# Kernel optimization log

Measured on AMD Instinct MI355X. Metric: run time of the kernel, lower is better.

## Reference

```python
import jax, jax.numpy as jnp
import numpy as np

BN_EPS = 1e-5


def _bn(h, gamma, beta, mean, var):
    return (h - mean) * jax.lax.rsqrt(var + BN_EPS) * gamma + beta


def _gin_conv(x, edge_index, edge_weight, Wa, ba, g, be, m, v, Wb, bb):
    # GINConv: (1+eps)*x + sum_j w_ij * x_j, eps=0; then MLP: Linear->BN->ReLU->Linear
    src, dst = edge_index[0], edge_index[1]
    msg = x[src] * edge_weight[:, None]                      # [E, C]
    agg = jax.ops.segment_sum(msg, dst, num_segments=x.shape[0])  # [N, C]
    h = x + agg
    h = h @ Wa + ba
    h = jax.nn.relu(_bn(h, g, be, m, v))
    return h @ Wb + bb


def setup_inputs() -> dict:
    key = jax.random.key(0)
    ks = jax.random.split(key, 16)
    N, E, C_IN, C_OUT, H = 100000, 1600000, 128, 64, 32
    x = jax.random.normal(ks[0], (N, C_IN), dtype=jnp.float32)
    edge_index = jax.random.randint(ks[1], (2, E), 0, N, dtype=jnp.int32)
    edge_weight = jax.random.uniform(ks[2], (E,), dtype=jnp.float32)
    s1 = 1.0 / np.sqrt(C_IN)
    s2 = 1.0 / np.sqrt(H)
    return {
        "x": x,
        "edge_weight": edge_weight,
        "W1a": jax.random.normal(ks[3], (C_IN, H), dtype=jnp.float32) * s1,
        "b1a": jnp.zeros((H,), jnp.float32),
        "g1": jnp.ones((H,), jnp.float32),
        "be1": jnp.zeros((H,), jnp.float32),
        "m1": jax.random.normal(ks[4], (H,), dtype=jnp.float32) * 0.1,
        "v1": jax.random.uniform(ks[5], (H,), dtype=jnp.float32) + 0.5,
        "W1b": jax.random.normal(ks[6], (H, H), dtype=jnp.float32) * s2,
        "b1b": jnp.zeros((H,), jnp.float32),
        "W2a": jax.random.normal(ks[7], (H, C_OUT), dtype=jnp.float32) * s2,
        "b2a": jnp.zeros((C_OUT,), jnp.float32),
        "g2": jnp.ones((C_OUT,), jnp.float32),
        "be2": jnp.zeros((C_OUT,), jnp.float32),
        "m2": jax.random.normal(ks[8], (C_OUT,), dtype=jnp.float32) * 0.1,
        "v2": jax.random.uniform(ks[9], (C_OUT,), dtype=jnp.float32) + 0.5,
        "W2b": jax.random.normal(ks[10], (C_OUT, C_OUT), dtype=jnp.float32) * (1.0 / np.sqrt(C_OUT)),
        "b2b": jnp.zeros((C_OUT,), jnp.float32),
        "edge_index": edge_index,
    }


def reference(x, edge_weight, W1a, b1a, g1, be1, m1, v1, W1b, b1b,
              W2a, b2a, g2, be2, m2, v2, W2b, b2b, edge_index):
    # eval mode: dropout(p=0.6) is identity, BN uses running stats
    h = jax.nn.relu(_gin_conv(x, edge_index, edge_weight,
                              W1a, b1a, g1, be1, m1, v1, W1b, b1b))
    out = _gin_conv(h, edge_index, edge_weight,
                    W2a, b2a, g2, be2, m2, v2, W2b, b2b)
    return out
```

## Files before the change

### kernel.cpp

```cpp
#include <hip/hip_runtime.h>


#define BN_EPS 1e-5f
#define BKT 128
#define BKT_SH 7
#define EPB 4096
#define MAXB 800
#define LDS_E 2560

__device__ __forceinline__ unsigned short f2bf(float f) {
    unsigned u = __float_as_uint(f);
    return (unsigned short)((u + 0x7FFFu + ((u >> 16) & 1u)) >> 16);
}
__device__ __forceinline__ float bflo(unsigned u) { return __uint_as_float(u << 16); }
__device__ __forceinline__ float bfhi(unsigned u) { return __uint_as_float(u & 0xFFFF0000u); }

__device__ __forceinline__ void gacc8(uint4 v, float w, float* acc) {
    acc[0] += bflo(v.x) * w; acc[1] += bfhi(v.x) * w;
    acc[2] += bflo(v.y) * w; acc[3] += bfhi(v.y) * w;
    acc[4] += bflo(v.z) * w; acc[5] += bfhi(v.z) * w;
    acc[6] += bflo(v.w) * w; acc[7] += bfhi(v.w) * w;
}

__device__ __forceinline__ void gather_seg8(const unsigned short* __restrict__ tab,
                                            const int2* __restrict__ epack,
                                            int e, int end, int c0, float* acc) {
    long long q0 = 0, q1 = 0, q2 = 0, q3 = 0;
    if (e + 4 <= end) {
        q0 = __builtin_nontemporal_load((const long long*)&epack[e + 0]);
        q1 = __builtin_nontemporal_load((const long long*)&epack[e + 1]);
        q2 = __builtin_nontemporal_load((const long long*)&epack[e + 2]);
        q3 = __builtin_nontemporal_load((const long long*)&epack[e + 3]);
    }
    for (; e + 8 <= end; e += 4) {
        int s0 = (int)q0, s1 = (int)q1, s2 = (int)q2, s3 = (int)q3;
        float w0 = __int_as_float((int)(q0 >> 32));
        float w1 = __int_as_float((int)(q1 >> 32));
        float w2 = __int_as_float((int)(q2 >> 32));
        float w3 = __int_as_float((int)(q3 >> 32));
        uint4 v0 = *(const uint4*)&tab[(size_t)s0 * 32 + c0];
        uint4 v1 = *(const uint4*)&tab[(size_t)s1 * 32 + c0];
        uint4 v2 = *(const uint4*)&tab[(size_t)s2 * 32 + c0];
        uint4 v3 = *(const uint4*)&tab[(size_t)s3 * 32 + c0];
        q0 = __builtin_nontemporal_load((const long long*)&epack[e + 4]);
        q1 = __builtin_nontemporal_load((const long long*)&epack[e + 5]);
        q2 = __builtin_nontemporal_load((const long long*)&epack[e + 6]);
        q3 = __builtin_nontemporal_load((const long long*)&epack[e + 7]);
        gacc8(v0, w0, acc); gacc8(v1, w1, acc);
        gacc8(v2, w2, acc); gacc8(v3, w3, acc);
    }
    if (e + 4 <= end) {
        int s0 = (int)q0, s1 = (int)q1, s2 = (int)q2, s3 = (int)q3;
        float w0 = __int_as_float((int)(q0 >> 32));
        float w1 = __int_as_float((int)(q1 >> 32));
        float w2 = __int_as_float((int)(q2 >> 32));
        float w3 = __int_as_float((int)(q3 >> 32));
        uint4 v0 = *(const uint4*)&tab[(size_t)s0 * 32 + c0];
        uint4 v1 = *(const uint4*)&tab[(size_t)s1 * 32 + c0];
        uint4 v2 = *(const uint4*)&tab[(size_t)s2 * 32 + c0];
        uint4 v3 = *(const uint4*)&tab[(size_t)s3 * 32 + c0];
        gacc8(v0, w0, acc); gacc8(v1, w1, acc);
        gacc8(v2, w2, acc); gacc8(v3, w3, acc);
        e += 4;
    }
    for (; e < end; ++e) {
        long long q = __builtin_nontemporal_load((const long long*)&epack[e]);
        int sn = (int)q;
        float w = __int_as_float((int)(q >> 32));
        uint4 v = *(const uint4*)&tab[(size_t)sn * 32 + c0];
        gacc8(v, w, acc);
    }
}

__global__ __launch_bounds__(256) void gemm1_kernel(const float* __restrict__ x,
                                                    const float* __restrict__ W,
                                                    unsigned short* __restrict__ y1b,
                                                    int* __restrict__ gcur,
                                                    int N, int ncur) {
    __shared__ float xs[64][129];
    __shared__ float ws[128 * 32];
    int t = threadIdx.x;
    if (t == 0) {
        int b0 = blockIdx.x * 16;
        #pragma unroll
        for (int j = 0; j < 16; ++j)
            if (b0 + j < ncur) gcur[b0 + j] = 0;
    }
    for (int i = t; i < 4096; i += 256) ws[i] = W[i];
    int row0 = blockIdx.x * 64;
    for (int j = 0; j < 8; ++j) {
        int f4 = t + j * 256;
        int r  = f4 >> 5;
        int kc = (f4 & 31) << 2;
        if (row0 + r < N) {
            float4 v = *(const float4*)&x[(size_t)(row0 + r) * 128 + kc];
            xs[r][kc + 0] = v.x; xs[r][kc + 1] = v.y;
            xs[r][kc + 2] = v.z; xs[r][kc + 3] = v.w;
        }
    }
    __syncthreads();
    int r  = t >> 2;
    int c0 = (t & 3) << 3;
    if (row0 + r >= N) return;
    float a[8] = {0.f, 0.f, 0.f, 0.f, 0.f, 0.f, 0.f, 0.f};
    #pragma unroll 8
    for (int k = 0; k < 128; ++k) {
        float xv = xs[r][k];
        const float* wr = &ws[k * 32 + c0];
        #pragma unroll
        for (int j = 0; j < 8; ++j) a[j] += xv * wr[j];
    }
    ushort4 o0 = {f2bf(a[0]), f2bf(a[1]), f2bf(a[2]), f2bf(a[3])};
    ushort4 o1 = {f2bf(a[4]), f2bf(a[5]), f2bf(a[6]), f2bf(a[7])};
    *(ushort4*)&y1b[(size_t)(row0 + r) * 32 + c0 + 0] = o0;
    *(ushort4*)&y1b[(size_t)(row0 + r) * 32 + c0 + 4] = o1;
}

__global__ __launch_bounds__(512) void stage_kernel(const int* __restrict__ ei,
                                                    const float* __restrict__ ew,
                                                    int* __restrict__ gcur,
                                                    int2* __restrict__ staged,
                                                    int E, int cap, int NBUCK) {
    __shared__ int hist[MAXB], base_[MAXB], curs[MAXB];
    __shared__ int gbase[MAXB];
    __shared__ int2 data[EPB];
    __shared__ unsigned short bslot[EPB];
    int t  = threadIdx.x;
    int e0 = blockIdx.x * EPB;
    int cnt = min(EPB, E - e0);
    for (int i = t; i < MAXB; i += 512) hist[i] = 0;
    __syncthreads();
    for (int i = t; i < cnt; i += 512) {
        int d = ei[(size_t)E + e0 + i];
        atomicAdd(&hist[d >> BKT_SH], 1);
    }
    __syncthreads();
    int lo = t * 2;
    int v0 = (lo + 0 < MAXB) ? hist[lo + 0] : 0;
    int v1 = (lo + 1 < MAXB) ? hist[lo + 1] : 0;
    int s = v0 + v1;
    gbase[t] = s;
    __syncthreads();
    for (int off = 1; off < 512; off <<= 1) {
        int y = (t >= off) ? gbase[t - off] : 0;
        __syncthreads();
        gbase[t] += y;
        __syncthreads();
    }
    int excl = gbase[t] - s;
    if (lo + 0 < MAXB) { base_[lo + 0] = excl; curs[lo + 0] = excl; }
    excl += v0;
    if (lo + 1 < MAXB) { base_[lo + 1] = excl; curs[lo + 1] = excl; }
    __syncthreads();
    for (int i = t; i < cnt; i += 512) {
        int sn = ei[e0 + i];
        int d  = ei[(size_t)E + e0 + i];
        float w = ew[e0 + i];
        int b = d >> BKT_SH, dl = d & (BKT - 1);
        int pos = atomicAdd(&curs[b], 1);
        data[pos]  = make_int2((dl << 20) | sn, __float_as_int(w));
        bslot[pos] = (unsigned short)b;
    }
    __syncthreads();
    for (int b = t; b < NBUCK; b += 512) {
        int c = hist[b];
        gbase[b] = c ? atomicAdd(&gcur[b * 16], c) : 0;
    }
    __syncthreads();
    for (int i = t; i < cnt; i += 512) {
        int b  = bslot[i];
        int gp = gbase[b] + (i - base_[b]);
        if (gp < cap) staged[(size_t)b * cap + gp] = data[i];
    }
}

__global__ __launch_bounds__(256) void refill_kernel(const int2* __restrict__ staged,
                                                     const int* __restrict__ gcur,
                                                     int2* __restrict__ epack,
                                                     int2* __restrict__ row_se,
                                                     int N, int cap) {
    __shared__ int2 ebuf[LDS_E];
    __shared__ int hist[BKT];
    __shared__ int curs[BKT];
    int b = blockIdx.x, t = threadIdx.x;
    int cnt  = min(gcur[b * 16], cap);
    int base = b * cap;
    size_t e0 = (size_t)b * cap;
    if (t < BKT) hist[t] = 0;
    __syncthreads();
    for (int i = t; i < cnt; i += 256) {
        int2 p = staged[e0 + i];
        ebuf[i] = p;
        atomicAdd(&hist[p.x >> 20], 1);
    }
    __syncthreads();
    if (t < BKT) curs[t] = hist[t];
    __syncthreads();
    for (int off = 1; off < BKT; off <<= 1) {
        int y = (t < BKT && t >= off) ? curs[t - off] : 0;
        __syncthreads();
        if (t < BKT) curs[t] += y;
        __syncthreads();
    }
    if (t < BKT) {
        int excl = curs[t] - hist[t];
        int node = (b << BKT_SH) + t;
        if (node < N) row_se[node] = make_int2(base + excl, base + excl + hist[t]);
        curs[t] = excl;
    }
    __syncthreads();
    for (int i = t; i < cnt; i += 256) {
        int2 p = ebuf[i];
        int dl = p.x >> 20;
        int pos = base + atomicAdd(&curs[dl], 1);
        epack[pos] = make_int2(p.x & 0xFFFFF, p.y);
    }
}

__global__ __launch_bounds__(256) void layer1_kernel(
    const unsigned short* __restrict__ y1b, const int2* __restrict__ row_se,
    const int2* __restrict__ epack,
    const float* __restrict__ b1a, const float* __restrict__ g1,
    const float* __restrict__ be1, const float* __restrict__ m1,
    const float* __restrict__ v1, const float* __restrict__ W1b,
    const float* __restrict__ b1b, unsigned short* __restrict__ h1b, int N) {
    __shared__ float w1b[1024];
    __shared__ float t1s[64][33];
    int t = threadIdx.x;
    for (int i = t; i < 1024; i += 256) w1b[i] = W1b[i];
    __syncthreads();
    int g = t >> 2, l = t & 3;
    int node = blockIdx.x * 64 + g;
    int c0 = l << 3;
    bool act = node < N;
    float acc[8] = {0.f, 0.f, 0.f, 0.f, 0.f, 0.f, 0.f, 0.f};
    if (act) {
        int2 se = row_se[node];
        gather_seg8(y1b, epack, se.x, se.y, c0, acc);
        uint4 sv = *(const uint4*)&y1b[(size_t)node * 32 + c0];
        gacc8(sv, 1.f, acc);
        #pragma unroll
        for (int j = 0; j < 8; ++j) {
            int c = c0 + j;
            float scale = g1[c] * rsqrtf(v1[c] + BN_EPS);
            t1s[g][c] = fmaxf((acc[j] + b1a[c] - m1[c]) * scale + be1[c], 0.f);
        }
    }
    asm volatile("" ::: "memory");
    if (act) {
        float a[8];
        #pragma unroll
        for (int j = 0; j < 8; ++j) a[j] = b1b[c0 + j];
        #pragma unroll
        for (int k = 0; k < 32; ++k) {
            float tv = t1s[g][k];
            const float* wr = &w1b[k * 32 + c0];
            #pragma unroll
            for (int j = 0; j < 8; ++j) a[j] += tv * wr[j];
        }
        unsigned long long p0 = 0, p1 = 0;
        #pragma unroll
        for (int j = 0; j < 4; ++j)
            p0 |= (unsigned long long)f2bf(fmaxf(a[j], 0.f)) << (16 * j);
        #pragma unroll
        for (int j = 0; j < 4; ++j)
            p1 |= (unsigned long long)f2bf(fmaxf(a[4 + j], 0.f)) << (16 * j);
        __builtin_nontemporal_store(p0, (unsigned long long*)&h1b[(size_t)node * 32 + c0 + 0]);
        __builtin_nontemporal_store(p1, (unsigned long long*)&h1b[(size_t)node * 32 + c0 + 4]);
    }
}

__global__ __launch_bounds__(256) void layer2a_kernel(
    const unsigned short* __restrict__ h1b, const int2* __restrict__ row_se,
    const int2* __restrict__ epack,
    const float* __restrict__ W2a, const float* __restrict__ b2a,
    const float* __restrict__ g2, const float* __restrict__ be2,
    const float* __restrict__ m2, const float* __restrict__ v2,
    unsigned short* __restrict__ t2b, int N) {
    __shared__ float w2a[2048];
    __shared__ float s1s[64][33];
    __shared__ float sc2s[64], sh2s[64];
    int t = threadIdx.x;
    for (int i = t; i < 2048; i += 256) w2a[i] = W2a[i];
    if (t < 64) {
        float sc = g2[t] * rsqrtf(v2[t] + BN_EPS);
        sc2s[t] = sc;
        sh2s[t] = (b2a[t] - m2[t]) * sc + be2[t];
    }
    __syncthreads();
    int g = t >> 2, l = t & 3;
    int node = blockIdx.x * 64 + g;
    int c0 = l << 3;
    bool act = node < N;
    float acc[8] = {0.f, 0.f, 0.f, 0.f, 0.f, 0.f, 0.f, 0.f};
    if (act) {
        int2 se = row_se[node];
        gather_seg8(h1b, epack, se.x, se.y, c0, acc);
        uint4 sv = *(const uint4*)&h1b[(size_t)node * 32 + c0];
        gacc8(sv, 1.f, acc);
        #pragma unroll
        for (int j = 0; j < 8; ++j) s1s[g][c0 + j] = acc[j];
    }
    asm volatile("" ::: "memory");
    if (act) {
        int d0 = l << 4;
        float a[16];
        #pragma unroll
        for (int j = 0; j < 16; ++j) a[j] = 0.f;
        #pragma unroll
        for (int k = 0; k < 32; ++k) {
            float sv = s1s[g][k];
            const float* wr = &w2a[k * 64 + d0];
            #pragma unroll
            for (int j = 0; j < 16; ++j) a[j] += sv * wr[j];
        }
        unsigned long long pk[4] = {0, 0, 0, 0};
        #pragma unroll
        for (int j = 0; j < 16; ++j) {
            int c = d0 + j;
            float o = fmaxf(a[j] * sc2s[c] + sh2s[c], 0.f);
            pk[j >> 2] |= (unsigned long long)f2bf(o) << (16 * (j & 3));
        }
        #pragma unroll
        for (int q = 0; q < 4; ++q)
            __builtin_nontemporal_store(pk[q],
                (unsigned long long*)&t2b[(size_t)node * 64 + d0 + 4 * q]);
    }
}

__global__ __launch_bounds__(256) void final_kernel(const unsigned short* __restrict__ t2b,
                                                    const float* __restrict__ W2b,
                                                    const float* __restrict__ b2b,
                                                    float* __restrict__ out, int N) {
    __shared__ float w2b[4096];
    __shared__ float t2s[32][68];
    int t = threadIdx.x;
    for (int i = t; i < 4096; i += 256) w2b[i] = W2b[i];
    int g = t >> 3, l = t & 7;
    int node = blockIdx.x * 32 + g;
    int c0 = l << 3;
    bool act = node < N;
    if (act) {
        uint4 v = *(const uint4*)&t2b[(size_t)node * 64 + c0];
        t2s[g][c0 + 0] = bflo(v.x); t2s[g][c0 + 1] = bfhi(v.x);
        t2s[g][c0 + 2] = bflo(v.y); t2s[g][c0 + 3] = bfhi(v.y);
        t2s[g][c0 + 4] = bflo(v.z); t2s[g][c0 + 5] = bfhi(v.z);
        t2s[g][c0 + 6] = bflo(v.w); t2s[g][c0 + 7] = bfhi(v.w);
    }
    __syncthreads();
    if (act) {
        float a[8];
        #pragma unroll
        for (int j = 0; j < 8; ++j) a[j] = b2b[c0 + j];
        #pragma unroll 8
        for (int k = 0; k < 64; ++k) {
            float tv = t2s[g][k];
            const float* wr = &w2b[k * 64 + c0];
            float4 w0 = *(const float4*)wr;
            float4 w1 = *(const float4*)(wr + 4);
            a[0] += tv * w0.x; a[1] += tv * w0.y; a[2] += tv * w0.z; a[3] += tv * w0.w;
            a[4] += tv * w1.x; a[5] += tv * w1.y; a[6] += tv * w1.z; a[7] += tv * w1.w;
        }
        *(float4*)&out[(size_t)node * 64 + c0 + 0] = *(float4*)&a[0];
        *(float4*)&out[(size_t)node * 64 + c0 + 4] = *(float4*)&a[4];
    }
}

extern "C" void kernel_launch(void* const* d_in, const int* in_sizes, int n_in,
                              void* d_out, int out_size, void* d_ws, size_t ws_size,
                              hipStream_t stream) {
    const float* x   = (const float*)d_in[0];
    const float* ew  = (const float*)d_in[1];
    const float* W1a = (const float*)d_in[2];
    const float* b1a = (const float*)d_in[3];
    const float* g1  = (const float*)d_in[4];
    const float* be1 = (const float*)d_in[5];
    const float* m1  = (const float*)d_in[6];
    const float* v1  = (const float*)d_in[7];
    const float* W1b = (const float*)d_in[8];
    const float* b1b = (const float*)d_in[9];
    const float* W2a = (const float*)d_in[10];
    const float* b2a = (const float*)d_in[11];
    const float* g2  = (const float*)d_in[12];
    const float* be2 = (const float*)d_in[13];
    const float* m2  = (const float*)d_in[14];
    const float* v2  = (const float*)d_in[15];
    const float* W2b = (const float*)d_in[16];
    const float* b2b = (const float*)d_in[17];
    const int*   ei  = (const int*)d_in[18];

    const int N = in_sizes[0] / 128;
    const int E = in_sizes[1];
    const int NBUCK = (N + BKT - 1) >> BKT_SH;
    const int NCUR  = NBUCK * 16;

    unsigned short* y1b = (unsigned short*)d_ws;
    int2*  row_se  = (int2*)(y1b + (size_t)N * 32);
    int*   gcur    = (int*)(row_se + N);
    int2*  epack   = (int2*)(gcur + NCUR + 16);
    size_t fixed_bytes = (char*)epack - (char*)d_ws;
    size_t avail = (ws_size > fixed_bytes) ? (ws_size - fixed_bytes) : 0;
    int cap = (int)((avail / (2 * sizeof(int2))) / NBUCK);
    cap &= ~63;
    if (cap > LDS_E) cap = LDS_E;
    int2* staged = epack + (size_t)NBUCK * cap;
    unsigned short* h1b = (unsigned short*)staged;
    unsigned short* t2b = h1b + (size_t)N * 32;

    gemm1_kernel<<<(N + 63) / 64, 256, 0, stream>>>(x, W1a, y1b, gcur, N, NCUR);
    stage_kernel<<<(E + EPB - 1) / EPB, 512, 0, stream>>>(ei, ew, gcur, staged, E, cap, NBUCK);
    refill_kernel<<<NBUCK, 256, 0, stream>>>(staged, gcur, epack, row_se, N, cap);
    layer1_kernel<<<(N + 63) / 64, 256, 0, stream>>>(y1b, row_se, epack,
                                                     b1a, g1, be1, m1, v1, W1b, b1b, h1b, N);
    layer2a_kernel<<<(N + 63) / 64, 256, 0, stream>>>(h1b, row_se, epack,
                                                      W2a, b2a, g2, be2, m2, v2, t2b, N);
    final_kernel<<<(N + 31) / 32, 256, 0, stream>>>(t2b, W2b, b2b, (float*)d_out, N);
}
```

Baseline: 166.8 us.

## Compute first-layer x@W1a projection with bf16 MFMA instead of scalar FMA

Replaces the LDS-tiled scalar fp32 GEMM in gemm1_kernel with MFMA 16x16x32 bf16 instructions. W is transposed and converted to bf16 in LDS, and x rows are loaded straight from global memory and converted to bf16 in registers. This drops the large x staging tile in LDS and the scalar inner loop. In exchange, inputs are rounded to bf16 before the multiply, which lowers precision. The output was already stored as bf16.

```diff
diff --git a/kernel.cpp b/kernel.cpp
--- a/kernel.cpp
+++ b/kernel.cpp
@@ -7,6 +7,9 @@
 #define EPB 4096
 #define MAXB 800
 #define LDS_E 2560
+
+typedef __attribute__((ext_vector_type(8))) short bf16x8;
+typedef __attribute__((ext_vector_type(4))) float f32x4v;
 
 __device__ __forceinline__ unsigned short f2bf(float f) {
     unsigned u = __float_as_uint(f);
@@ -77,8 +80,7 @@
                                                     unsigned short* __restrict__ y1b,
                                                     int* __restrict__ gcur,
                                                     int N, int ncur) {
-    __shared__ float xs[64][129];
-    __shared__ float ws[128 * 32];
+    __shared__ unsigned short wbT[32][136];
     int t = threadIdx.x;
     if (t == 0) {
         int b0 = blockIdx.x * 16;
@@ -86,34 +88,46 @@
         for (int j = 0; j < 16; ++j)
             if (b0 + j < ncur) gcur[b0 + j] = 0;
     }
-    for (int i = t; i < 4096; i += 256) ws[i] = W[i];
-    int row0 = blockIdx.x * 64;
-    for (int j = 0; j < 8; ++j) {
-        int f4 = t + j * 256;
-        int r  = f4 >> 5;
-        int kc = (f4 & 31) << 2;
-        if (row0 + r < N) {
-            float4 v = *(const float4*)&x[(size_t)(row0 + r) * 128 + kc];
-            xs[r][kc + 0] = v.x; xs[r][kc + 1] = v.y;
-            xs[r][kc + 2] = v.z; xs[r][kc + 3] = v.w;
-        }
-    }
-    __syncthreads();
-    int r  = t >> 2;
-    int c0 = (t & 3) << 3;
-    if (row0 + r >= N) return;
-    float a[8] = {0.f, 0.f, 0.f, 0.f, 0.f, 0.f, 0.f, 0.f};
-    #pragma unroll 8
-    for (int k = 0; k < 128; ++k) {
-        float xv = xs[r][k];
-        const float* wr = &ws[k * 32 + c0];
-        #pragma unroll
-        for (int j = 0; j < 8; ++j) a[j] += xv * wr[j];
-    }
-    ushort4 o0 = {f2bf(a[0]), f2bf(a[1]), f2bf(a[2]), f2bf(a[3])};
-    ushort4 o1 = {f2bf(a[4]), f2bf(a[5]), f2bf(a[6]), f2bf(a[7])};
-    *(ushort4*)&y1b[(size_t)(row0 + r) * 32 + c0 + 0] = o0;
-    *(ushort4*)&y1b[(size_t)(row0 + r) * 32 + c0 + 4] = o1;
+    for (int i = t; i < 4096; i += 256) {
+        int k = i >> 5, c = i & 31;
+        wbT[c][k] = f2bf(W[i]);
+    }
+    __syncthreads();
+    int wid = t >> 6, lane = t & 63;
+    int lr = lane & 15, lg = lane >> 4;
+    int arow = blockIdx.x * 64 + wid * 16 + lr;
+    int xr = min(arow, N - 1);
+    bf16x8 bf[4][2];
+    #pragma unroll
+    for (int s = 0; s < 4; ++s) {
+        int kb = s * 32 + lg * 8;
+        bf[s][0] = *(const bf16x8*)&wbT[lr][kb];
+        bf[s][1] = *(const bf16x8*)&wbT[16 + lr][kb];
+    }
+    f32x4v acc0 = {0.f, 0.f, 0.f, 0.f};
+    f32x4v acc1 = {0.f, 0.f, 0.f, 0.f};
+    #pragma unroll
+    for (int s = 0; s < 4; ++s) {
+        const float* xp = &x[(size_t)xr * 128 + s * 32 + lg * 8];
+        float4 xa = *(const float4*)xp;
+        float4 xb = *(const float4*)(xp + 4);
+        bf16x8 af;
+        af[0] = (short)f2bf(xa.x); af[1] = (short)f2bf(xa.y);
+        af[2] = (short)f2bf(xa.z); af[3] = (short)f2bf(xa.w);
+        af[4] = (short)f2bf(xb.x); af[5] = (short)f2bf(xb.y);
+        af[6] = (short)f2bf(xb.z); af[7] = (short)f2bf(xb.w);
+        acc0 = __builtin_amdgcn_mfma_f32_16x16x32_bf16(af, bf[s][0], acc0, 0, 0, 0);
+        acc1 = __builtin_amdgcn_mfma_f32_16x16x32_bf16(af, bf[s][1], acc1, 0, 0, 0);
+    }
+    int rowbase = blockIdx.x * 64 + wid * 16 + lg * 4;
+    #pragma unroll
+    for (int r = 0; r < 4; ++r) {
+        int orow = rowbase + r;
+        if (orow < N) {
+            y1b[(size_t)orow * 32 + lr]      = f2bf(acc0[r]);
+            y1b[(size_t)orow * 32 + 16 + lr] = f2bf(acc1[r]);
+        }
+    }
 }
 
 __global__ __launch_bounds__(512) void stage_kernel(const int* __restrict__ ei,
```

New measurement: 149.5 us. 10.4% less time.
